# Optimization experiments

Measured on AMD Instinct MI355X. Metric: run time of the kernel, lower is better.

Reference implementation:

```python
import jax, jax.numpy as jnp
import numpy as np

N_HEAD = 16
ROPE_BASE = 10000.0


def _rope_cache(T, head_dim):
    # half-split RoPE: cos/sin of shape [T, head_dim//2]
    half = head_dim // 2
    inv_freq = ROPE_BASE ** (-jnp.arange(half, dtype=jnp.float32) / half)
    angles = jnp.arange(T, dtype=jnp.float32)[:, None] * inv_freq[None, :]  # [T, half]
    return jnp.cos(angles), jnp.sin(angles)


def _apply_rope(x, cos, sin):
    # x: [B, H, T, D]; cos/sin: [T, D//2]
    half = x.shape[-1] // 2
    x1, x2 = x[..., :half], x[..., half:]
    c = cos[None, None, :, :]
    s = sin[None, None, :, :]
    return jnp.concatenate([x1 * c - x2 * s, x1 * s + x2 * c], axis=-1)


def setup_inputs() -> dict:
    key = jax.random.key(0)
    k1, k2, k3 = jax.random.split(key, 3)
    B, T, C = 2, 2048, 1024
    x = jax.random.normal(k1, (B, T, C), dtype=jnp.float32)
    w_attn = jax.random.normal(k2, (C, 3 * C), dtype=jnp.float32) * (C ** -0.5)
    b_attn = jnp.zeros((3 * C,), dtype=jnp.float32)
    w_proj = jax.random.normal(k3, (C, C), dtype=jnp.float32) * (C ** -0.5)
    b_proj = jnp.zeros((C,), dtype=jnp.float32)
    return {"x": x, "w_attn": w_attn, "b_attn": b_attn, "w_proj": w_proj, "b_proj": b_proj}


def reference(x, w_attn, b_attn, w_proj, b_proj):
    B, T, C = x.shape
    H = N_HEAD
    hd = C // H

    qkv = x @ w_attn + b_attn                      # [B, T, 3C] fused QKV
    q, k, v = jnp.split(qkv, 3, axis=-1)
    q = q.reshape(B, T, H, hd).transpose(0, 2, 1, 3)  # [B, H, T, hd]
    k = k.reshape(B, T, H, hd).transpose(0, 2, 1, 3)
    v = v.reshape(B, T, H, hd).transpose(0, 2, 1, 3)

    cos, sin = _rope_cache(T, hd)
    q = _apply_rope(q, cos, sin)
    k = _apply_rope(k, cos, sin)

    scale = 1.0 / jnp.sqrt(jnp.float32(hd))
    att = jnp.einsum("bhqd,bhkd->bhqk", q, k) * scale  # [B, H, T, T]
    causal = jnp.tril(jnp.ones((T, T), dtype=bool))
    att = jnp.where(causal[None, None], att, -jnp.inf)
    att = jax.nn.softmax(att, axis=-1)
    y = jnp.einsum("bhqk,bhkd->bhqd", att, v)          # [B, H, T, hd]
    y = y.transpose(0, 2, 1, 3).reshape(B, T, C)
    return y @ w_proj + b_proj
```

## Files before the change

### kernel.cpp

```cpp
#include <hip/hip_runtime.h>
#include <hip/hip_bf16.h>
#include <cmath>

typedef _Float16 half_t;
typedef half_t half4 __attribute__((ext_vector_type(4)));
typedef half_t half8 __attribute__((ext_vector_type(8)));
typedef float f32x4 __attribute__((ext_vector_type(4)));

#define N_HEADS 16
#define HD      64
#define T_SEQ   2048
#define B_SZ    2
#define C_DIM   1024
#define M_ROWS  (B_SZ * T_SEQ)
#define N_QKV   (3 * C_DIM)
#define QSCALE  0.18033688f

__device__ inline void load_lds16(const half_t* g, half_t* l) {
  __builtin_amdgcn_global_load_lds(
      (const __attribute__((address_space(1))) void*)g,
      (__attribute__((address_space(3))) void*)l, 16, 0, 0);
}

__global__ __launch_bounds__(256) void k_prep(const float* __restrict__ x,
                                              half_t* __restrict__ xb,
                                              const float* __restrict__ wa,
                                              half_t* __restrict__ wT,
                                              const float* __restrict__ wp,
                                              half_t* __restrict__ wpT) {
  __shared__ float tile[64][65];
  int bid = blockIdx.x, tid = threadIdx.x;
  if (bid < 4096) {
    int i = (bid * 256 + tid) * 4;
    float4 v = *(const float4*)(x + i);
    half_t o[4] = {(half_t)v.x, (half_t)v.y, (half_t)v.z, (half_t)v.w};
    *(ulong1*)(xb + i) = *(ulong1*)o;
    return;
  }
  const float* in; half_t* out; int K, N, id;
  if (bid < 4096 + 768) { id = bid - 4096; in = wa; out = wT;  K = 1024; N = 3072; }
  else                  { id = bid - 4864; in = wp; out = wpT; K = 1024; N = 1024; }
  int n0 = (id % (N / 64)) * 64, k0 = (id / (N / 64)) * 64;
  int tx = tid & 63, ty = tid >> 6;
  #pragma unroll
  for (int i = 0; i < 64; i += 4)
    tile[ty + i][tx] = in[(size_t)(k0 + ty + i) * N + n0 + tx];
  __syncthreads();
  #pragma unroll
  for (int i = 0; i < 64; i += 4) {
    int r = ty + i;
    out[(size_t)(n0 + r) * K + k0 + tx] = (half_t)tile[tx][r];
  }
}

template <typename OT, int TN>
__global__ __launch_bounds__(256) void k_gemm(const half_t* __restrict__ A,
                                              const half_t* __restrict__ Bt,
                                              const float* __restrict__ bias,
                                              OT* __restrict__ C,
                                              int M, int N, int K) {
  constexpr int NI = TN / 32;
  __shared__ half_t As[128 * 64];
  __shared__ half_t Bs[TN * 64];
  int tid = threadIdx.x;
  int wave = tid >> 6, lane = tid & 63;
  int lane15 = lane & 15, quad = lane >> 4;
  int wm = (wave >> 1) * 64, wn = (wave & 1) * (TN / 2);
  int bm0 = blockIdx.y * 128, bn0 = blockIdx.x * TN;
  f32x4 acc[4][NI] = {};

  for (int kb = 0; kb < K; kb += 64) {
    const half_t* Ag = A + (size_t)bm0 * K + kb;
    const half_t* Bg = Bt + (size_t)bn0 * K + kb;
    __syncthreads();
    #pragma unroll
    for (int p = 0; p < 4; p++) {
      int fc = wave * 4 * 64 + p * 64 + lane;
      int r = fc >> 3, c = (fc & 7) ^ (r & 7);
      load_lds16(Ag + (size_t)r * K + c * 8, As + (wave * 4 + p) * 512);
    }
    #pragma unroll
    for (int p = 0; p < NI; p++) {
      int fc = wave * NI * 64 + p * 64 + lane;
      int r = fc >> 3, c = (fc & 7) ^ (r & 7);
      load_lds16(Bg + (size_t)r * K + c * 8, Bs + (wave * NI + p) * 512);
    }
    __syncthreads();
    #pragma unroll
    for (int ks = 0; ks < 2; ks++) {
      half8 af[4], bf[NI];
      #pragma unroll
      for (int i = 0; i < 4; i++) {
        int Ra = wm + i * 16 + lane15;
        af[i] = *(const half8*)(As + Ra * 64 + ((ks * 4 + quad) ^ (Ra & 7)) * 8);
      }
      #pragma unroll
      for (int i = 0; i < NI; i++) {
        int Rb = wn + i * 16 + lane15;
        bf[i] = *(const half8*)(Bs + Rb * 64 + ((ks * 4 + quad) ^ (Rb & 7)) * 8);
      }
      #pragma unroll
      for (int mi = 0; mi < 4; mi++)
        #pragma unroll
        for (int ni = 0; ni < NI; ni++)
          acc[mi][ni] = __builtin_amdgcn_mfma_f32_16x16x32_f16(af[mi], bf[ni], acc[mi][ni], 0, 0, 0);
    }
  }
  #pragma unroll
  for (int mi = 0; mi < 4; mi++)
    #pragma unroll
    for (int ni = 0; ni < NI; ni++) {
      int n = bn0 + wn + ni * 16 + lane15;
      float bv = bias[n];
      int mrow = bm0 + wm + mi * 16 + quad * 4;
      #pragma unroll
      for (int r = 0; r < 4; r++)
        C[(size_t)(mrow + r) * N + n] = (OT)(acc[mi][ni][r] + bv);
    }
}

__global__ __launch_bounds__(256) void k_rope(const half_t* __restrict__ qkv,
                                              half_t* __restrict__ Q,
                                              half_t* __restrict__ Ko,
                                              half_t* __restrict__ Vt) {
  __shared__ float vt[64][65];
  int bh = blockIdx.y;
  int b = bh >> 4, h = bh & 15;
  int t0 = blockIdx.x * 64;
  int tid = threadIdx.x;
  int trow = tid >> 5, i = tid & 31;
  float inv = exp2f(-(float)i * (13.287712379549449f / 32.0f));
  #pragma unroll
  for (int p = 0; p < 8; p++) {
    int tloc = p * 8 + trow;
    int t = t0 + tloc;
    const half_t* row = qkv + (size_t)(b * T_SEQ + t) * N_QKV;
    float q1 = (float)row[h * 64 + i],        q2 = (float)row[h * 64 + i + 32];
    float k1 = (float)row[1024 + h * 64 + i], k2 = (float)row[1024 + h * 64 + i + 32];
    float v1 = (float)row[2048 + h * 64 + i], v2 = (float)row[2048 + h * 64 + i + 32];
    float s, c;
    sincosf((float)t * inv, &s, &c);
    size_t base = ((size_t)bh * T_SEQ + t) * HD;
    Q[base + i]       = (half_t)((q1 * c - q2 * s) * QSCALE);
    Q[base + i + 32]  = (half_t)((q1 * s + q2 * c) * QSCALE);
    Ko[base + i]      = (half_t)(k1 * c - k2 * s);
    Ko[base + i + 32] = (half_t)(k1 * s + k2 * c);
    vt[i][tloc]      = v1;
    vt[i + 32][tloc] = v2;
  }
  __syncthreads();
  int d = tid >> 6, tc = tid & 63;
  #pragma unroll
  for (int p = 0; p < 16; p++) {
    int dd = p * 4 + d;
    Vt[((size_t)bh * HD + dd) * T_SEQ + t0 + tc] = (half_t)vt[dd][tc];
  }
}

__device__ __forceinline__ void sched_noop() {}

template <bool DIAG>
__device__ __forceinline__ void tile_mfma(const half_t* __restrict__ Kt,
                                          const half_t* __restrict__ Vt,
                                          half8 bq0, half8 bq1,
                                          f32x4 (&ot)[4], float& l,
                                          int lane15, int quad, int qloc) {
  f32x4 sacc[4];
  #pragma unroll
  for (int s = 0; s < 4; s++) {
    int R_ = s * 16 + lane15;
    half8 ak0 = *(const half8*)(Kt + R_ * 64 + ((quad) ^ (R_ & 7)) * 8);
    half8 ak1 = *(const half8*)(Kt + R_ * 64 + ((4 + quad) ^ (R_ & 7)) * 8);
    f32x4 z = {};
    z = __builtin_amdgcn_mfma_f32_16x16x32_f16(ak0, bq0, z, 0, 0, 0);
    sacc[s] = __builtin_amdgcn_mfma_f32_16x16x32_f16(ak1, bq1, z, 0, 0, 0);
  }
  #pragma unroll
  for (int s = 0; s < 4; s++) {
    half4 bp;
    #pragma unroll
    for (int r = 0; r < 4; r++) {
      float sv = sacc[s][r];
      if (DIAG && (s * 16 + quad * 4 + r > qloc)) sv = -1.0e30f;
      float p = exp2f(fminf(sv, 14.0f));
      l += p;
      bp[r] = (half_t)p;
    }
    #pragma unroll
    for (int nm = 0; nm < 4; nm++) {
      int Rv = nm * 16 + lane15;
      half4 av = *(const half4*)(Vt + Rv * 64 +
                                 ((2 * s + (quad >> 1)) ^ (Rv & 7)) * 8 +
                                 (quad & 1) * 4);
      ot[nm] = __builtin_amdgcn_mfma_f32_16x16x16f16(av, bp, ot[nm], 0, 0, 0);
    }
  }
}

#define STAGE2(bb, j0, j1)                                                     \
  {                                                                            \
    int fc = wave * 64 + lane;                                                 \
    int rr_ = fc >> 3, cc = (fc & 7) ^ (rr_ & 7);                              \
    load_lds16(Kb + (size_t)((j0) * 64 + rr_) * HD + cc * 8,                   \
               &Ks[bb][0][0] + fc * 8);                                        \
    load_lds16(Kb + (size_t)((j1) * 64 + rr_) * HD + cc * 8,                   \
               &Ks[bb][1][0] + fc * 8);                                        \
    load_lds16(Vb + (size_t)rr_ * T_SEQ + (j0) * 64 + cc * 8,                  \
               &Vs[bb][0][0] + fc * 8);                                        \
    load_lds16(Vb + (size_t)rr_ * T_SEQ + (j1) * 64 + cc * 8,                  \
               &Vs[bb][1][0] + fc * 8);                                        \
  }

__device__ __forceinline__ void process_tile(
    int qt, const half_t* __restrict__ Qb, const half_t* __restrict__ Kb,
    const half_t* __restrict__ Vb, half_t* __restrict__ y, int b, int h,
    half_t (&Ks)[2][2][4096], half_t (&Vs)[2][2][4096],
    int wave, int lane, int g, int wq, int lane15, int quad) {
  int q0 = qt * 64;
  int qrow = q0 + wq * 16 + lane15;
  half8 bq0 = *(const half8*)(Qb + (size_t)qrow * HD + quad * 8);
  half8 bq1 = *(const half8*)(Qb + (size_t)qrow * HD + 32 + quad * 8);
  f32x4 ot[4] = {};
  float l = 0.f;
  int R = (qt + 2) >> 1;
  for (int r = 0; r < R - 1; r++) {
    __syncthreads();
    int nj = 2 * (r + 1);
    int nj1 = (nj + 1 <= qt) ? nj + 1 : qt;
    STAGE2((r + 1) & 1, nj, nj1);
    tile_mfma<false>(&Ks[r & 1][g][0], &Vs[r & 1][g][0], bq0, bq1, ot, l,
                     lane15, quad, 0);
  }
  __syncthreads();
  {
    int jtl = 2 * (R - 1) + g;
    const half_t* Kt = &Ks[(R - 1) & 1][g][0];
    const half_t* Vt = &Vs[(R - 1) & 1][g][0];
    if (jtl == qt)
      tile_mfma<true>(Kt, Vt, bq0, bq1, ot, l, lane15, quad, wq * 16 + lane15);
    else if (jtl < qt)
      tile_mfma<false>(Kt, Vt, bq0, bq1, ot, l, lane15, quad, 0);
  }
  l += __shfl_xor(l, 16);
  l += __shfl_xor(l, 32);
  __syncthreads();
  float* cb = (float*)&Ks[0][0][0];
  int ci = (wq * 64 + lane) * 17;
  if (g == 1) {
    #pragma unroll
    for (int nm = 0; nm < 4; nm++)
      #pragma unroll
      for (int r = 0; r < 4; r++) cb[ci + nm * 4 + r] = ot[nm][r];
    cb[ci + 16] = l;
  }
  __syncthreads();
  if (g == 0) {
    #pragma unroll
    for (int nm = 0; nm < 4; nm++)
      #pragma unroll
      for (int r = 0; r < 4; r++) ot[nm][r] += cb[ci + nm * 4 + r];
    l += cb[ci + 16];
    float invl = 1.0f / l;
    int t = q0 + wq * 16 + lane15;
    half_t* yr = y + (size_t)(b * T_SEQ + t) * C_DIM + h * 64;
    #pragma unroll
    for (int nm = 0; nm < 4; nm++) {
      half4 o4;
      #pragma unroll
      for (int r = 0; r < 4; r++) o4[r] = (half_t)(ot[nm][r] * invl);
      *(half4*)(yr + nm * 16 + quad * 4) = o4;
    }
  }
  __syncthreads();
}

__global__ __launch_bounds__(512) void k_flash(const half_t* __restrict__ Qg,
                                               const half_t* __restrict__ Kg,
                                               const half_t* __restrict__ Vg,
                                               half_t* __restrict__ y) {
  __shared__ half_t Ks[2][2][4096];
  __shared__ half_t Vs[2][2][4096];
  int bh = blockIdx.y;
  int b = bh >> 4, h = bh & 15;
  int x = blockIdx.x;
  int tid = threadIdx.x;
  int wave = tid >> 6, lane = tid & 63;
  int g = wave >> 2, wq = wave & 3;
  int lane15 = lane & 15, quad = lane >> 4;
  const half_t* Qb = Qg + (size_t)bh * T_SEQ * HD;
  const half_t* Kb = Kg + (size_t)bh * T_SEQ * HD;
  const half_t* Vb = Vg + (size_t)bh * HD * T_SEQ;

  int qtA = x, qtB = 31 - x;
  STAGE2(0, 0, (qtA >= 1 ? 1 : 0));
  process_tile(qtA, Qb, Kb, Vb, y, b, h, Ks, Vs, wave, lane, g, wq, lane15, quad);
  STAGE2(0, 0, 1);
  process_tile(qtB, Qb, Kb, Vb, y, b, h, Ks, Vs, wave, lane, g, wq, lane15, quad);
  #undef STAGE2
}

extern "C" void kernel_launch(void* const* d_in, const int* in_sizes, int n_in,
                              void* d_out, int out_size, void* d_ws, size_t ws_size,
                              hipStream_t stream) {
  const float* x      = (const float*)d_in[0];
  const float* w_attn = (const float*)d_in[1];
  const float* b_attn = (const float*)d_in[2];
  const float* w_proj = (const float*)d_in[3];
  const float* b_proj = (const float*)d_in[4];
  float* out = (float*)d_out;

  char* ws = (char*)d_ws;
  const size_t MB = 1u << 20;
  half_t* xb  = (half_t*)(ws);
  half_t* wT  = (half_t*)(ws + 8 * MB);
  half_t* wpT = (half_t*)(ws + 14 * MB);
  half_t* Q   = (half_t*)(ws + 16 * MB);
  half_t* Kb  = (half_t*)(ws + 24 * MB);
  half_t* Vt  = (half_t*)(ws + 32 * MB);
  half_t* qkv = (half_t*)(ws + 40 * MB);
  half_t* y   = (half_t*)(ws + 40 * MB);

  k_prep<<<4096 + 768 + 256, 256, 0, stream>>>(x, xb, w_attn, wT, w_proj, wpT);
  k_gemm<half_t, 128><<<dim3(N_QKV / 128, M_ROWS / 128), 256, 0, stream>>>(
      xb, wT, b_attn, qkv, M_ROWS, N_QKV, C_DIM);
  k_rope<<<dim3(T_SEQ / 64, B_SZ * N_HEADS), 256, 0, stream>>>(qkv, Q, Kb, Vt);
  k_flash<<<dim3(16, B_SZ * N_HEADS), 512, 0, stream>>>(Q, Kb, Vt, y);
  k_gemm<float, 64><<<dim3(C_DIM / 64, M_ROWS / 128), 256, 0, stream>>>(
      y, wpT, b_proj, out, M_ROWS, C_DIM, C_DIM);
}
```

Baseline: 194.4 us.

## Double flash-attention query tile to 128 rows with 1024-thread blocks

The causal attention kernel now gives each block 128-row query tiles and runs 16 waves (8 query-row waves × 2 key halves) per block. Each staging step loads one 128-key K/V chunk into LDS, so every loaded K/V tile serves twice as many query rows and the number of barrier-separated iterations per query tile drops. The grid is halved to 8×32 blocks and still pairs tiles qt and 15-qt for causal load balance. In exchange, 1024-thread blocks with a launch-bounds hint constrain registers per thread, and the diagonal step now does more masked work.

After: 185.1 us. -4.8%, faster.

```diff
diff --git a/kernel.cpp b/kernel.cpp
--- a/kernel.cpp
+++ b/kernel.cpp
@@ -157,8 +157,6 @@
   }
 }
 
-__device__ __forceinline__ void sched_noop() {}
-
 template <bool DIAG>
 __device__ __forceinline__ void tile_mfma(const half_t* __restrict__ Kt,
                                           const half_t* __restrict__ Vt,
@@ -197,54 +195,51 @@
   }
 }
 
-#define STAGE2(bb, j0, j1)                                                     \
+#define STAGE(bb, t_)                                                          \
   {                                                                            \
-    int fc = wave * 64 + lane;                                                 \
-    int rr_ = fc >> 3, cc = (fc & 7) ^ (rr_ & 7);                              \
-    load_lds16(Kb + (size_t)((j0) * 64 + rr_) * HD + cc * 8,                   \
-               &Ks[bb][0][0] + fc * 8);                                        \
-    load_lds16(Kb + (size_t)((j1) * 64 + rr_) * HD + cc * 8,                   \
-               &Ks[bb][1][0] + fc * 8);                                        \
-    load_lds16(Vb + (size_t)rr_ * T_SEQ + (j0) * 64 + cc * 8,                  \
-               &Vs[bb][0][0] + fc * 8);                                        \
-    load_lds16(Vb + (size_t)rr_ * T_SEQ + (j1) * 64 + cc * 8,                  \
-               &Vs[bb][1][0] + fc * 8);                                        \
+    int gS = wave >> 3;                                                        \
+    int idx = (wave & 7) * 64 + lane;                                          \
+    int rr_ = idx >> 3, cc = (idx & 7) ^ (rr_ & 7);                            \
+    int j = 2 * (t_) + gS;                                                     \
+    load_lds16(Kb + (size_t)(j * 64 + rr_) * HD + cc * 8,                      \
+               &KV[bb][0][gS][0] + idx * 8);                                   \
+    load_lds16(Vb + (size_t)rr_ * T_SEQ + j * 64 + cc * 8,                     \
+               &KV[bb][1][gS][0] + idx * 8);                                   \
   }
 
 __device__ __forceinline__ void process_tile(
     int qt, const half_t* __restrict__ Qb, const half_t* __restrict__ Kb,
     const half_t* __restrict__ Vb, half_t* __restrict__ y, int b, int h,
-    half_t (&Ks)[2][2][4096], half_t (&Vs)[2][2][4096],
+    half_t (&KV)[2][2][2][4096],
     int wave, int lane, int g, int wq, int lane15, int quad) {
-  int q0 = qt * 64;
+  int q0 = qt * 128;
   int qrow = q0 + wq * 16 + lane15;
   half8 bq0 = *(const half8*)(Qb + (size_t)qrow * HD + quad * 8);
   half8 bq1 = *(const half8*)(Qb + (size_t)qrow * HD + 32 + quad * 8);
   f32x4 ot[4] = {};
   float l = 0.f;
-  int R = (qt + 2) >> 1;
+  int R = qt + 1;
   for (int r = 0; r < R - 1; r++) {
     __syncthreads();
-    int nj = 2 * (r + 1);
-    int nj1 = (nj + 1 <= qt) ? nj + 1 : qt;
-    STAGE2((r + 1) & 1, nj, nj1);
-    tile_mfma<false>(&Ks[r & 1][g][0], &Vs[r & 1][g][0], bq0, bq1, ot, l,
+    STAGE((r + 1) & 1, r + 1);
+    tile_mfma<false>(&KV[r & 1][0][g][0], &KV[r & 1][1][g][0], bq0, bq1, ot, l,
                      lane15, quad, 0);
   }
   __syncthreads();
   {
-    int jtl = 2 * (R - 1) + g;
-    const half_t* Kt = &Ks[(R - 1) & 1][g][0];
-    const half_t* Vt = &Vs[(R - 1) & 1][g][0];
-    if (jtl == qt)
+    int buf = (R - 1) & 1;
+    const half_t* Kt = &KV[buf][0][g][0];
+    const half_t* Vt = &KV[buf][1][g][0];
+    if (g == 0)
       tile_mfma<true>(Kt, Vt, bq0, bq1, ot, l, lane15, quad, wq * 16 + lane15);
-    else if (jtl < qt)
-      tile_mfma<false>(Kt, Vt, bq0, bq1, ot, l, lane15, quad, 0);
+    else if (wq >= 4)
+      tile_mfma<true>(Kt, Vt, bq0, bq1, ot, l, lane15, quad,
+                      (wq - 4) * 16 + lane15);
   }
   l += __shfl_xor(l, 16);
   l += __shfl_xor(l, 32);
   __syncthreads();
-  float* cb = (float*)&Ks[0][0][0];
+  float* cb = (float*)&KV[0][0][0][0];
   int ci = (wq * 64 + lane) * 17;
   if (g == 1) {
     #pragma unroll
@@ -274,29 +269,28 @@
   __syncthreads();
 }
 
-__global__ __launch_bounds__(512) void k_flash(const half_t* __restrict__ Qg,
-                                               const half_t* __restrict__ Kg,
-                                               const half_t* __restrict__ Vg,
-                                               half_t* __restrict__ y) {
-  __shared__ half_t Ks[2][2][4096];
-  __shared__ half_t Vs[2][2][4096];
+__global__ __launch_bounds__(1024, 4) void k_flash(const half_t* __restrict__ Qg,
+                                                   const half_t* __restrict__ Kg,
+                                                   const half_t* __restrict__ Vg,
+                                                   half_t* __restrict__ y) {
+  __shared__ half_t KV[2][2][2][4096];
   int bh = blockIdx.y;
   int b = bh >> 4, h = bh & 15;
   int x = blockIdx.x;
   int tid = threadIdx.x;
   int wave = tid >> 6, lane = tid & 63;
-  int g = wave >> 2, wq = wave & 3;
+  int g = wave >> 3, wq = wave & 7;
   int lane15 = lane & 15, quad = lane >> 4;
   const half_t* Qb = Qg + (size_t)bh * T_SEQ * HD;
   const half_t* Kb = Kg + (size_t)bh * T_SEQ * HD;
   const half_t* Vb = Vg + (size_t)bh * HD * T_SEQ;
 
-  int qtA = x, qtB = 31 - x;
-  STAGE2(0, 0, (qtA >= 1 ? 1 : 0));
-  process_tile(qtA, Qb, Kb, Vb, y, b, h, Ks, Vs, wave, lane, g, wq, lane15, quad);
-  STAGE2(0, 0, 1);
-  process_tile(qtB, Qb, Kb, Vb, y, b, h, Ks, Vs, wave, lane, g, wq, lane15, quad);
-  #undef STAGE2
+  int qtA = x, qtB = 15 - x;
+  STAGE(0, 0);
+  process_tile(qtA, Qb, Kb, Vb, y, b, h, KV, wave, lane, g, wq, lane15, quad);
+  STAGE(0, 0);
+  process_tile(qtB, Qb, Kb, Vb, y, b, h, KV, wave, lane, g, wq, lane15, quad);
+  #undef STAGE
 }
 
 extern "C" void kernel_launch(void* const* d_in, const int* in_sizes, int n_in,
@@ -324,7 +318,7 @@
   k_gemm<half_t, 128><<<dim3(N_QKV / 128, M_ROWS / 128), 256, 0, stream>>>(
       xb, wT, b_attn, qkv, M_ROWS, N_QKV, C_DIM);
   k_rope<<<dim3(T_SEQ / 64, B_SZ * N_HEADS), 256, 0, stream>>>(qkv, Q, Kb, Vt);
-  k_flash<<<dim3(16, B_SZ * N_HEADS), 512, 0, stream>>>(Q, Kb, Vt, y);
+  k_flash<<<dim3(8, B_SZ * N_HEADS), 1024, 0, stream>>>(Q, Kb, Vt, y);
   k_gemm<float, 64><<<dim3(C_DIM / 64, M_ROWS / 128), 256, 0, stream>>>(
       y, wpT, b_proj, out, M_ROWS, C_DIM, C_DIM);
 }
```
